# Performance work log

Hardware: AMD Instinct MI355X
Metric: run time of the kernel (lower is better)

The kernel has to match this reference:

```python
import jax, jax.numpy as jnp
import numpy as np

N, IN, H, C = 100000, 128, 4, 64  # nodes, in_channels, heads, out_channels
E0 = 1600000
NEG_SLOPE = 0.2


def setup_inputs() -> dict:
    key = jax.random.key(0)
    ks = jax.random.split(key, 8)
    x = jax.random.normal(ks[0], (N, IN), dtype=jnp.float32)
    edge_index = jax.random.randint(ks[1], (2, E0), 0, N, dtype=jnp.int64)
    s = 1.0 / np.sqrt(IN)
    W = jax.random.uniform(ks[2], (IN, H * C), jnp.float32, -s, s)
    att_src = jax.random.normal(ks[3], (H, C), jnp.float32) * 0.1
    att_dst = jax.random.normal(ks[4], (H, C), jnp.float32) * 0.1
    bias = jnp.zeros((C,), jnp.float32)
    sf = 1.0 / np.sqrt(C)
    fc_w = jax.random.uniform(ks[5], (C, 1), jnp.float32, -sf, sf)
    fc_b = jax.random.uniform(ks[6], (1,), jnp.float32, -sf, sf)
    return {"x": x, "edge_index": edge_index, "W": W, "att_src": att_src,
            "att_dst": att_dst, "bias": bias, "fc_w": fc_w, "fc_b": fc_b}


def gat_forward(x, edge_index, W, att_src, att_dst, bias, fc_w, fc_b):
    n = x.shape[0]
    # add self-loops (PyG GATConv default)
    loops = jnp.arange(n, dtype=edge_index.dtype)
    src = jnp.concatenate([edge_index[0], loops])
    dst = jnp.concatenate([edge_index[1], loops])

    h = (x @ W).reshape(n, H, C)                     # [N,H,C]
    a_src = jnp.einsum('nhc,hc->nh', h, att_src)     # [N,H]
    a_dst = jnp.einsum('nhc,hc->nh', h, att_dst)

    logits = jax.nn.leaky_relu(a_src[src] + a_dst[dst], NEG_SLOPE)  # [E,H]
    m = jax.ops.segment_max(logits, dst, num_segments=n)            # [N,H]
    e = jnp.exp(logits - m[dst])
    z = jax.ops.segment_sum(e, dst, num_segments=n)                 # [N,H]
    alpha = e / (z[dst] + 1e-16)                                    # [E,H]

    msgs = h[src] * alpha[:, :, None]                               # [E,H,C]
    out = jax.ops.segment_sum(msgs, dst, num_segments=n)            # [N,H,C]
    out = out.mean(axis=1) + bias                                   # concat=False -> head mean

    out = jax.nn.relu(out)
    return jax.nn.sigmoid(out @ fc_w + fc_b)                        # [N,1]


def reference(x, edge_index, W, att_src, att_dst, bias, fc_w, fc_b):
    return gat_forward(x, edge_index, W, att_src, att_dst, bias, fc_w, fc_b)
```

## Files before the change

kernel.cpp:

```cpp
#include <hip/hip_runtime.h>


#define NN 100000
#define IN_DIM 128
#define HC 256
#define NEG_SLOPE 0.2f
#define SCAN_CHUNK 1024

typedef __attribute__((ext_vector_type(8))) __bf16 bf16x8;
typedef __attribute__((ext_vector_type(4))) float f32x4;
typedef __attribute__((ext_vector_type(2))) float f32x2;

__device__ __forceinline__ unsigned short f2bf(float f) {
  unsigned int u = __builtin_bit_cast(unsigned int, f);
  u += 0x7fffu + ((u >> 16) & 1u);
  return (unsigned short)(u >> 16);
}
__device__ __forceinline__ float bf_lo(unsigned int v) {
  return __builtin_bit_cast(float, v << 16);
}
__device__ __forceinline__ float bf_hi(unsigned int v) {
  return __builtin_bit_cast(float, v & 0xffff0000u);
}

__global__ __launch_bounds__(256) void k_gemm(const float* __restrict__ x,
    const float* __restrict__ W, const float* __restrict__ att_src,
    const float* __restrict__ att_dst, unsigned char* __restrict__ h8,
    float* __restrict__ a_src, float* __restrict__ a_dst,
    int* __restrict__ deg, int n_tiles) {
  __shared__ unsigned short wt[256 * 128];
  const int tid = threadIdx.x;
  {
    const int gti = blockIdx.x * 256 + tid;
    if (gti < NN) deg[gti] = 0;
  }
  {
    const int c = tid;
    const int swz = (c & 7) << 3;
    #pragma unroll 4
    for (int i = 0; i < 64; ++i) {
      float w0 = W[(2 * i) * HC + c];
      float w1 = W[(2 * i + 1) * HC + c];
      unsigned int pk = (unsigned int)f2bf(w0) | ((unsigned int)f2bf(w1) << 16);
      int kidx = (2 * i) ^ swz;
      *(unsigned int*)&wt[c * 128 + kidx] = pk;
    }
  }
  __syncthreads();
  const int wave = tid >> 6, lane = tid & 63;
  const int g = lane >> 4, i16 = lane & 15;
  float as_l[16], ad_l[16];
  #pragma unroll
  for (int nt = 0; nt < 16; ++nt) {
    as_l[nt] = att_src[nt * 16 + i16];
    ad_l[nt] = att_dst[nt * 16 + i16];
  }
  for (int t = blockIdx.x; t < n_tiles; t += gridDim.x) {
    const int rbase = t * 64 + wave * 16;
    int arow = rbase + i16; if (arow >= NN) arow = NN - 1;
    const float* xp = x + (size_t)arow * IN_DIM;
    f32x4 acc[16];
    #pragma unroll
    for (int nt = 0; nt < 16; ++nt) acc[nt] = (f32x4){0.f, 0.f, 0.f, 0.f};
    #pragma unroll
    for (int kk = 0; kk < 4; ++kk) {
      const int k0 = kk * 32 + g * 8;
      f32x4 xa = *(const f32x4*)(xp + k0);
      f32x4 xb = *(const f32x4*)(xp + k0 + 4);
      bf16x8 af;
      af[0] = (__bf16)xa[0]; af[1] = (__bf16)xa[1];
      af[2] = (__bf16)xa[2]; af[3] = (__bf16)xa[3];
      af[4] = (__bf16)xb[0]; af[5] = (__bf16)xb[1];
      af[6] = (__bf16)xb[2]; af[7] = (__bf16)xb[3];
      #pragma unroll
      for (int nt = 0; nt < 16; ++nt) {
        const int col = nt * 16 + i16;
        const bf16x8 bf = *(const bf16x8*)&wt[col * 128 + (k0 ^ ((col & 7) << 3))];
        acc[nt] = __builtin_amdgcn_mfma_f32_16x16x32_bf16(af, bf, acc[nt], 0, 0, 0);
      }
    }
    f32x4 ps[4], pd[4];
    #pragma unroll
    for (int r = 0; r < 4; ++r) {
      ps[r] = (f32x4){0.f, 0.f, 0.f, 0.f};
      pd[r] = (f32x4){0.f, 0.f, 0.f, 0.f};
    }
    #pragma unroll
    for (int nt = 0; nt < 16; ++nt) {
      const int hh = nt >> 2;
      #pragma unroll
      for (int r = 0; r < 4; ++r) {
        ps[r][hh] += acc[nt][r] * as_l[nt];
        pd[r][hh] += acc[nt][r] * ad_l[nt];
      }
    }
    #pragma unroll
    for (int r = 0; r < 4; ++r) {
      #pragma unroll
      for (int hh = 0; hh < 4; ++hh) {
        #pragma unroll
        for (int d = 1; d <= 8; d <<= 1) {
          ps[r][hh] += __shfl_xor(ps[r][hh], d);
          pd[r][hh] += __shfl_xor(pd[r][hh], d);
        }
      }
    }
    if (i16 == 0) {
      #pragma unroll
      for (int r = 0; r < 4; ++r) {
        const int row = rbase + g * 4 + r;
        if (row < NN) {
          *(f32x4*)(a_src + (size_t)row * 4) = ps[r];
          *(f32x4*)(a_dst + (size_t)row * 4) = pd[r];
        }
      }
    }
    #pragma unroll
    for (int r = 0; r < 4; ++r) {
      const int row = rbase + g * 4 + r;
      if (row < NN) {
        unsigned char* hp = h8 + (size_t)row * HC + i16;
        #pragma unroll
        for (int nt = 0; nt < 16; ++nt) {
          unsigned int pv = __builtin_amdgcn_cvt_pk_fp8_f32(acc[nt][r], acc[nt][r], 0, false);
          hp[nt * 16] = (unsigned char)pv;
        }
      }
    }
  }
}

__global__ void k_rank(const int* __restrict__ ei, int* __restrict__ deg,
                       int* __restrict__ rank, int e0) {
  int e = blockIdx.x * 256 + threadIdx.x;
  if (e < e0) rank[e] = atomicAdd(&deg[ei[e0 + e]], 1);
}
__global__ __launch_bounds__(256) void k_scan1(const int* __restrict__ deg,
                                               int* __restrict__ bsum) {
  __shared__ int sm[256];
  const int b = blockIdx.x, t = threadIdx.x;
  const int base = b * SCAN_CHUNK + t * 4;
  int s = 0;
  #pragma unroll
  for (int r = 0; r < 4; ++r) { int e = base + r; if (e < NN) s += deg[e] + 1; }
  sm[t] = s; __syncthreads();
  for (int off = 128; off > 0; off >>= 1) {
    if (t < off) sm[t] += sm[t + off];
    __syncthreads();
  }
  if (t == 0) bsum[b] = sm[0];
}
__global__ __launch_bounds__(128) void k_scan2(const int* __restrict__ bsum,
                                               int* __restrict__ boff, int nb) {
  __shared__ int sm[128];
  const int t = threadIdx.x;
  sm[t] = (t < nb) ? bsum[t] : 0; __syncthreads();
  for (int off = 1; off < 128; off <<= 1) {
    int v = (t >= off) ? sm[t - off] : 0;
    __syncthreads();
    sm[t] += v;
    __syncthreads();
  }
  if (t < nb) boff[t] = (t == 0) ? 0 : sm[t - 1];
}
__global__ __launch_bounds__(256) void k_scan3(const int* __restrict__ deg,
    const int* __restrict__ boff, int* __restrict__ rowptr, int etot) {
  __shared__ int sm[256];
  const int b = blockIdx.x, t = threadIdx.x;
  const int base = b * SCAN_CHUNK + t * 4;
  int v[4]; int s = 0;
  #pragma unroll
  for (int r = 0; r < 4; ++r) {
    int e = base + r;
    v[r] = (e < NN) ? deg[e] + 1 : 0;
    s += v[r];
  }
  sm[t] = s; __syncthreads();
  for (int off = 1; off < 256; off <<= 1) {
    int u = (t >= off) ? sm[t - off] : 0;
    __syncthreads();
    sm[t] += u;
    __syncthreads();
  }
  int excl = boff[b] + sm[t] - s;
  #pragma unroll
  for (int r = 0; r < 4; ++r) {
    int e = base + r;
    if (e < NN) rowptr[e] = excl;
    excl += v[r];
  }
  if (b == 0 && t == 0) rowptr[NN] = etot;
}
__global__ void k_scatter(const int* __restrict__ ei,
    const float* __restrict__ a_src, const float* __restrict__ a_dst,
    const int* __restrict__ rank, const int* __restrict__ rowptr,
    uint4* __restrict__ rec, int e0) {
  int idx = blockIdx.x * 256 + threadIdx.x;
  if (idx >= e0 + NN) return;
  int s, d, pos;
  if (idx < e0) {
    s = ei[idx]; d = ei[e0 + idx];
    pos = rowptr[d] + 1 + rank[idx];
  } else {
    s = d = idx - e0;
    pos = rowptr[d];
  }
  const f32x4 as4 = *(const f32x4*)(a_src + (size_t)s * 4);
  const f32x4 ad4 = *(const f32x4*)(a_dst + (size_t)d * 4);
  float ev[4];
  #pragma unroll
  for (int h = 0; h < 4; ++h) {
    float lg = as4[h] + ad4[h];
    lg = lg > 0.f ? lg : NEG_SLOPE * lg;
    ev[h] = __expf(lg);
  }
  uint4 r;
  r.x = (unsigned int)s;
  r.y = (unsigned int)f2bf(ev[0]) | ((unsigned int)f2bf(ev[1]) << 16);
  r.z = (unsigned int)f2bf(ev[2]) | ((unsigned int)f2bf(ev[3]) << 16);
  r.w = 0;
  rec[pos] = r;
}

__global__ __launch_bounds__(256) void k_main(const unsigned char* __restrict__ h8,
    const uint4* __restrict__ rec, const int* __restrict__ rowptr,
    const float* __restrict__ bias, const float* __restrict__ fc_w,
    const float* __restrict__ fc_b, float* __restrict__ out) {
  const int tid = threadIdx.x, lane = tid & 63;
  const int n = blockIdx.x * 4 + (tid >> 6);
  const int eh = lane >> 5;
  const int c8 = lane & 31;
  const int head = c8 >> 3;
  const float wz = ((c8 & 7) == 0) ? 1.f : 0.f;
  const unsigned char* __restrict__ hb = h8 + c8 * 8;
  const int beg = rowptr[n], end = rowptr[n + 1];

  float a0 = 0.f, a1 = 0.f, a2 = 0.f, a3 = 0.f;
  float a4 = 0.f, a5 = 0.f, a6 = 0.f, a7 = 0.f;
  float zl = 0.f;
  int b0 = beg;
  const int bend = beg + ((end - beg) & ~7);
  for (; b0 < bend; b0 += 8) {
    #pragma unroll
    for (int u = 0; u < 4; ++u) {
      const uint4 r = rec[b0 + u * 2 + eh];
      const unsigned int evw = (head & 2) ? r.z : r.y;
      const float ev = (head & 1) ? bf_hi(evw) : bf_lo(evw);
      zl += wz * ev;
      const uint2 hv = *(const uint2*)(hb + ((size_t)r.x << 8));
      const f32x2 f01 = __builtin_amdgcn_cvt_pk_f32_fp8(hv.x, false);
      const f32x2 f23 = __builtin_amdgcn_cvt_pk_f32_fp8(hv.x, true);
      const f32x2 f45 = __builtin_amdgcn_cvt_pk_f32_fp8(hv.y, false);
      const f32x2 f67 = __builtin_amdgcn_cvt_pk_f32_fp8(hv.y, true);
      a0 += ev * f01[0]; a1 += ev * f01[1];
      a2 += ev * f23[0]; a3 += ev * f23[1];
      a4 += ev * f45[0]; a5 += ev * f45[1];
      a6 += ev * f67[0]; a7 += ev * f67[1];
    }
  }
  for (; b0 < end; b0 += 2) {
    const int idx = b0 + eh;
    const bool v = idx < end;
    const uint4 r = rec[v ? idx : beg];
    const unsigned int evw = (head & 2) ? r.z : r.y;
    float ev = (head & 1) ? bf_hi(evw) : bf_lo(evw);
    ev = v ? ev : 0.f;
    zl += wz * ev;
    const uint2 hv = *(const uint2*)(hb + ((size_t)r.x << 8));
    const f32x2 f01 = __builtin_amdgcn_cvt_pk_f32_fp8(hv.x, false);
    const f32x2 f23 = __builtin_amdgcn_cvt_pk_f32_fp8(hv.x, true);
    const f32x2 f45 = __builtin_amdgcn_cvt_pk_f32_fp8(hv.y, false);
    const f32x2 f67 = __builtin_amdgcn_cvt_pk_f32_fp8(hv.y, true);
    a0 += ev * f01[0]; a1 += ev * f01[1];
    a2 += ev * f23[0]; a3 += ev * f23[1];
    a4 += ev * f45[0]; a5 += ev * f45[1];
    a6 += ev * f67[0]; a7 += ev * f67[1];
  }
  a0 += __shfl_xor(a0, 32); a1 += __shfl_xor(a1, 32);
  a2 += __shfl_xor(a2, 32); a3 += __shfl_xor(a3, 32);
  a4 += __shfl_xor(a4, 32); a5 += __shfl_xor(a5, 32);
  a6 += __shfl_xor(a6, 32); a7 += __shfl_xor(a7, 32);
  zl += __shfl_xor(zl, 32);
  zl += __shfl_xor(zl, 1); zl += __shfl_xor(zl, 2); zl += __shfl_xor(zl, 4);
  const float rz = 0.25f / (zl + 1e-16f);
  a0 *= rz; a1 *= rz; a2 *= rz; a3 *= rz;
  a4 *= rz; a5 *= rz; a6 *= rz; a7 *= rz;
  a0 += __shfl_xor(a0, 8); a0 += __shfl_xor(a0, 16);
  a1 += __shfl_xor(a1, 8); a1 += __shfl_xor(a1, 16);
  a2 += __shfl_xor(a2, 8); a2 += __shfl_xor(a2, 16);
  a3 += __shfl_xor(a3, 8); a3 += __shfl_xor(a3, 16);
  a4 += __shfl_xor(a4, 8); a4 += __shfl_xor(a4, 16);
  a5 += __shfl_xor(a5, 8); a5 += __shfl_xor(a5, 16);
  a6 += __shfl_xor(a6, 8); a6 += __shfl_xor(a6, 16);
  a7 += __shfl_xor(a7, 8); a7 += __shfl_xor(a7, 16);

  const int ch0 = (c8 & 7) * 8;
  const f32x4 bv0 = *(const f32x4*)(bias + ch0);
  const f32x4 bv1 = *(const f32x4*)(bias + ch0 + 4);
  const f32x4 wv0 = *(const f32x4*)(fc_w + ch0);
  const f32x4 wv1 = *(const f32x4*)(fc_w + ch0 + 4);
  float p = fmaxf(a0 + bv0[0], 0.f) * wv0[0] + fmaxf(a1 + bv0[1], 0.f) * wv0[1]
          + fmaxf(a2 + bv0[2], 0.f) * wv0[2] + fmaxf(a3 + bv0[3], 0.f) * wv0[3]
          + fmaxf(a4 + bv1[0], 0.f) * wv1[0] + fmaxf(a5 + bv1[1], 0.f) * wv1[1]
          + fmaxf(a6 + bv1[2], 0.f) * wv1[2] + fmaxf(a7 + bv1[3], 0.f) * wv1[3];
  p += __shfl_xor(p, 1); p += __shfl_xor(p, 2); p += __shfl_xor(p, 4);
  if (lane == 0) out[n] = 1.f / (1.f + __expf(-(p + fc_b[0])));
}

extern "C" void kernel_launch(void* const* d_in, const int* in_sizes, int n_in,
                              void* d_out, int out_size, void* d_ws, size_t ws_size,
                              hipStream_t stream) {
  const float* x       = (const float*)d_in[0];
  const int*   ei      = (const int*)d_in[1];
  const float* W       = (const float*)d_in[2];
  const float* att_src = (const float*)d_in[3];
  const float* att_dst = (const float*)d_in[4];
  const float* bias    = (const float*)d_in[5];
  const float* fc_w    = (const float*)d_in[6];
  const float* fc_b    = (const float*)d_in[7];
  float* out = (float*)d_out;
  const int e0   = in_sizes[1] / 2;
  const int etot = e0 + NN;

  char* ws = (char*)d_ws;
  size_t off = 0;
  auto carve = [&](size_t bytes) {
    void* p = ws + off;
    off = (off + bytes + 255) & ~(size_t)255;
    return p;
  };
  unsigned char* h8 = (unsigned char*)carve((size_t)NN * HC);
  float* a_src = (float*)carve((size_t)NN * 4 * 4);
  float* a_dst = (float*)carve((size_t)NN * 4 * 4);
  int* deg     = (int*)carve((size_t)NN * 4);
  int* rowptr  = (int*)carve((size_t)(NN + 1) * 4);
  int* bsum    = (int*)carve(512);
  int* boff    = (int*)carve(512);
  int* rankb   = (int*)carve((size_t)e0 * 4);
  uint4* rec   = (uint4*)carve((size_t)etot * 16);

  const int n_tiles = (NN + 63) / 64;
  k_gemm<<<dim3(512), dim3(256), 0, stream>>>(x, W, att_src, att_dst,
                                              h8, a_src, a_dst, deg, n_tiles);
  k_rank<<<dim3((e0 + 255) / 256), dim3(256), 0, stream>>>(ei, deg, rankb, e0);
  const int nb = (NN + SCAN_CHUNK - 1) / SCAN_CHUNK;
  k_scan1<<<dim3(nb), dim3(256), 0, stream>>>(deg, bsum);
  k_scan2<<<dim3(1), dim3(128), 0, stream>>>(bsum, boff, nb);
  k_scan3<<<dim3(nb), dim3(256), 0, stream>>>(deg, boff, rowptr, etot);
  k_scatter<<<dim3((etot + 255) / 256), dim3(256), 0, stream>>>(ei, a_src, a_dst,
                                                                rankb, rowptr, rec, e0);
  k_main<<<dim3(25000), dim3(256), 0, stream>>>(h8, rec, rowptr,
                                                bias, fc_w, fc_b, out);
}
```

Measured before the change: 346.5 us.

## Store only source indices in CSR and compute attention weights in gather kernel

The scatter kernel now writes a 4-byte source index per edge instead of a 16-byte record holding the source and bf16 exp values, so it no longer gathers a_src/a_dst or evaluates exp. The main kernel reads a_dst once per node and, per edge, gathers a_src for its head and computes leaky-relu and exp in fp32. This cuts scatter write traffic and CSR read bandwidth but adds a random a_src gather and an exp per lane in the hot loop. The main kernel is also split into three launches over node ranges, with a bounds check added.

```diff
diff --git a/kernel.cpp b/kernel.cpp
--- a/kernel.cpp
+++ b/kernel.cpp
@@ -15,12 +15,6 @@
   unsigned int u = __builtin_bit_cast(unsigned int, f);
   u += 0x7fffu + ((u >> 16) & 1u);
   return (unsigned short)(u >> 16);
-}
-__device__ __forceinline__ float bf_lo(unsigned int v) {
-  return __builtin_bit_cast(float, v << 16);
-}
-__device__ __forceinline__ float bf_hi(unsigned int v) {
-  return __builtin_bit_cast(float, v & 0xffff0000u);
 }
 
 __global__ __launch_bounds__(256) void k_gemm(const float* __restrict__ x,
@@ -192,48 +186,36 @@
   if (b == 0 && t == 0) rowptr[NN] = etot;
 }
 __global__ void k_scatter(const int* __restrict__ ei,
-    const float* __restrict__ a_src, const float* __restrict__ a_dst,
     const int* __restrict__ rank, const int* __restrict__ rowptr,
-    uint4* __restrict__ rec, int e0) {
+    int* __restrict__ csr, int e0) {
   int idx = blockIdx.x * 256 + threadIdx.x;
   if (idx >= e0 + NN) return;
-  int s, d, pos;
+  int s, pos;
   if (idx < e0) {
-    s = ei[idx]; d = ei[e0 + idx];
-    pos = rowptr[d] + 1 + rank[idx];
+    s = ei[idx];
+    pos = rowptr[ei[e0 + idx]] + 1 + rank[idx];
   } else {
-    s = d = idx - e0;
-    pos = rowptr[d];
-  }
-  const f32x4 as4 = *(const f32x4*)(a_src + (size_t)s * 4);
-  const f32x4 ad4 = *(const f32x4*)(a_dst + (size_t)d * 4);
-  float ev[4];
-  #pragma unroll
-  for (int h = 0; h < 4; ++h) {
-    float lg = as4[h] + ad4[h];
-    lg = lg > 0.f ? lg : NEG_SLOPE * lg;
-    ev[h] = __expf(lg);
-  }
-  uint4 r;
-  r.x = (unsigned int)s;
-  r.y = (unsigned int)f2bf(ev[0]) | ((unsigned int)f2bf(ev[1]) << 16);
-  r.z = (unsigned int)f2bf(ev[2]) | ((unsigned int)f2bf(ev[3]) << 16);
-  r.w = 0;
-  rec[pos] = r;
+    s = idx - e0;
+    pos = rowptr[s];
+  }
+  csr[pos] = s;
 }
 
 __global__ __launch_bounds__(256) void k_main(const unsigned char* __restrict__ h8,
-    const uint4* __restrict__ rec, const int* __restrict__ rowptr,
+    const float* __restrict__ a_src, const float* __restrict__ a_dst,
+    const int* __restrict__ rowptr, const int* __restrict__ csr,
     const float* __restrict__ bias, const float* __restrict__ fc_w,
-    const float* __restrict__ fc_b, float* __restrict__ out) {
+    const float* __restrict__ fc_b, float* __restrict__ out, int n0) {
   const int tid = threadIdx.x, lane = tid & 63;
-  const int n = blockIdx.x * 4 + (tid >> 6);
+  const int n = n0 + blockIdx.x * 4 + (tid >> 6);
+  if (n >= NN) return;
   const int eh = lane >> 5;
   const int c8 = lane & 31;
   const int head = c8 >> 3;
   const float wz = ((c8 & 7) == 0) ? 1.f : 0.f;
   const unsigned char* __restrict__ hb = h8 + c8 * 8;
   const int beg = rowptr[n], end = rowptr[n + 1];
+  const float adh = a_dst[n * 4 + head];
 
   float a0 = 0.f, a1 = 0.f, a2 = 0.f, a3 = 0.f;
   float a4 = 0.f, a5 = 0.f, a6 = 0.f, a7 = 0.f;
@@ -243,11 +225,12 @@
   for (; b0 < bend; b0 += 8) {
     #pragma unroll
     for (int u = 0; u < 4; ++u) {
-      const uint4 r = rec[b0 + u * 2 + eh];
-      const unsigned int evw = (head & 2) ? r.z : r.y;
-      const float ev = (head & 1) ? bf_hi(evw) : bf_lo(evw);
+      const int sv = csr[b0 + u * 2 + eh];
+      float lg = a_src[sv * 4 + head] + adh;
+      lg = fmaxf(lg, NEG_SLOPE * lg);
+      const float ev = __expf(lg);
       zl += wz * ev;
-      const uint2 hv = *(const uint2*)(hb + ((size_t)r.x << 8));
+      const uint2 hv = *(const uint2*)(hb + ((size_t)sv << 8));
       const f32x2 f01 = __builtin_amdgcn_cvt_pk_f32_fp8(hv.x, false);
       const f32x2 f23 = __builtin_amdgcn_cvt_pk_f32_fp8(hv.x, true);
       const f32x2 f45 = __builtin_amdgcn_cvt_pk_f32_fp8(hv.y, false);
@@ -261,12 +244,12 @@
   for (; b0 < end; b0 += 2) {
     const int idx = b0 + eh;
     const bool v = idx < end;
-    const uint4 r = rec[v ? idx : beg];
-    const unsigned int evw = (head & 2) ? r.z : r.y;
-    float ev = (head & 1) ? bf_hi(evw) : bf_lo(evw);
-    ev = v ? ev : 0.f;
+    const int sv = csr[v ? idx : beg];
+    float lg = a_src[sv * 4 + head] + adh;
+    lg = fmaxf(lg, NEG_SLOPE * lg);
+    float ev = v ? __expf(lg) : 0.f;
     zl += wz * ev;
-    const uint2 hv = *(const uint2*)(hb + ((size_t)r.x << 8));
+    const uint2 hv = *(const uint2*)(hb + ((size_t)sv << 8));
     const f32x2 f01 = __builtin_amdgcn_cvt_pk_f32_fp8(hv.x, false);
     const f32x2 f23 = __builtin_amdgcn_cvt_pk_f32_fp8(hv.x, true);
     const f32x2 f45 = __builtin_amdgcn_cvt_pk_f32_fp8(hv.y, false);
@@ -337,7 +320,7 @@
   int* bsum    = (int*)carve(512);
   int* boff    = (int*)carve(512);
   int* rankb   = (int*)carve((size_t)e0 * 4);
-  uint4* rec   = (uint4*)carve((size_t)etot * 16);
+  int* csrbuf  = (int*)carve((size_t)etot * 4);
 
   const int n_tiles = (NN + 63) / 64;
   k_gemm<<<dim3(512), dim3(256), 0, stream>>>(x, W, att_src, att_dst,
@@ -347,8 +330,13 @@
   k_scan1<<<dim3(nb), dim3(256), 0, stream>>>(deg, bsum);
   k_scan2<<<dim3(1), dim3(128), 0, stream>>>(bsum, boff, nb);
   k_scan3<<<dim3(nb), dim3(256), 0, stream>>>(deg, boff, rowptr, etot);
-  k_scatter<<<dim3((etot + 255) / 256), dim3(256), 0, stream>>>(ei, a_src, a_dst,
-                                                                rankb, rowptr, rec, e0);
-  k_main<<<dim3(25000), dim3(256), 0, stream>>>(h8, rec, rowptr,
-                                                bias, fc_w, fc_b, out);
-}
+  k_scatter<<<dim3((etot + 255) / 256), dim3(256), 0, stream>>>(ei, rankb, rowptr,
+                                                                csrbuf, e0);
+  const int third = 8334;
+  k_main<<<dim3(third), dim3(256), 0, stream>>>(h8, a_src, a_dst, rowptr, csrbuf,
+                                                bias, fc_w, fc_b, out, 0);
+  k_main<<<dim3(third), dim3(256), 0, stream>>>(h8, a_src, a_dst, rowptr, csrbuf,
+                                                bias, fc_w, fc_b, out, 33336);
+  k_main<<<dim3(8333), dim3(256), 0, stream>>>(h8, a_src, a_dst, rowptr, csrbuf,
+                                               bias, fc_w, fc_b, out, 66672);
+}
```

Result: no change. 343.0 us (-1.0%).
